# Optimization experiments

Measured on AMD Instinct MI355X. Metric: run time of the kernel, lower is better.

## Reference

```python
import jax, jax.numpy as jnp
import numpy as np

K = 3            # kernel size
C_IN = 8
C_OUT = 16
PATCH = C_IN * K * K  # 72
EPS = 1e-6


def setup_inputs() -> dict:
    key = jax.random.key(0)
    k1, k2, k3 = jax.random.split(key, 3)
    in_tensor = jax.random.normal(k1, (4, C_IN, 112, 112), dtype=jnp.float32)
    # 1x1-conv weighting predictor: C_in -> PATCH*C_OUT channels
    w_pred = jax.random.normal(k2, (PATCH * C_OUT, C_IN), dtype=jnp.float32) * 0.05
    b_pred = jax.random.normal(k3, (PATCH * C_OUT,), dtype=jnp.float32) * 0.05
    return {"in_tensor": in_tensor, "w_pred": w_pred, "b_pred": b_pred}


def reference(in_tensor, w_pred, b_pred):
    B, C, H, W = in_tensor.shape
    # --- weighting module: predict dynamic weights per spatial location ---
    raw = jnp.einsum('bchw,oc->bohw', in_tensor, w_pred) + b_pred[None, :, None, None]
    weightings = raw.reshape(B, PATCH, C_OUT, H, W)          # [B, C*k*k, C_out, H, W]
    # norm = L2 norm of the dynamic weight over the patch dim -> [B, C_out, H, W]
    norm = jnp.sqrt(jnp.sum(weightings * weightings, axis=1)) + EPS
    # --- unfold: overlapping k x k patches, same padding, stride 1 ---
    patches = jax.lax.conv_general_dilated_patches(
        in_tensor, (K, K), (1, 1), 'SAME')                   # [B, C*k*k, H, W]
    # --- weighted sum over the patch dim, then normalize ---
    activations = jnp.einsum('bphw,bpohw->bohw', patches, weightings)  # [B, C_out, H, W]
    return activations / norm
```

## Files before the change

kernel.cpp:

```cpp
#include <hip/hip_runtime.h>
#include <math.h>

#define IMG_W 112
#define HW    12544
#define CI    8
#define CO    16
#define NP2   36
#define EPS   1e-6f

typedef __attribute__((ext_vector_type(8))) short short8;
typedef __attribute__((ext_vector_type(16))) float f32x16;

static __device__ inline short f2bf(float f) {
  unsigned u = __float_as_uint(f);
  return (short)((u + 0x7FFFu + ((u >> 16) & 1u)) >> 16);
}

static constexpr int DQ[9] = {-113, -112, -111, -1, 0, 1, 111, 112, 113};

__global__ __launch_bounds__(256, 3) void coda_mfma(
    const float* __restrict__ in, const float* __restrict__ wp,
    const float* __restrict__ bp, float* __restrict__ out)
{
  __shared__ short sA[NP2][2][32][8];
  __shared__ float sBuf[CI * 290];

  const int tid = threadIdx.x;
  const int b   = blockIdx.x / 196;
  const int r0  = (blockIdx.x - b * 196) * 64;
  const float* __restrict__ inb = in + b * CI * HW;

  for (int idx = tid; idx < NP2 * 64; idx += 256) {
    const int p2 = idx >> 6, l = idx & 63, ah = l >> 5, m = l & 31;
    const int row = p2 * 32 + m;
    short8 v = {0, 0, 0, 0, 0, 0, 0, 0};
    if (ah == 0) {
      const float* wr = wp + row * CI;
#pragma unroll
      for (int j = 0; j < 8; ++j) v[j] = f2bf(wr[j]);
    } else {
      v[0] = f2bf(bp[row]);
    }
    *(short8*)&sA[p2][ah][m][0] = v;
  }
  for (int k = tid; k < CI * 290; k += 256) {
    const int c = k / 290;
    const int i = k - c * 290;
    int gg = r0 - 113 + i;
    gg = (gg < 0) ? 0 : (gg > HW - 1 ? HW - 1 : gg);
    sBuf[k] = inb[c * HW + gg];
  }
  __syncthreads();

  const int wave = tid >> 6;
  const int lane = tid & 63;
  const int g    = wave & 1;
  const int hh   = wave >> 1;
  const int ln   = lane & 31;
  const int hi   = lane >> 5;
  const int px   = r0 + g * 32 + ln;
  const int hrow = px / IMG_W;
  const int wcol = px - hrow * IMG_W;
  const int off  = g * 32 + ln + 113;

  float vm[9];
#pragma unroll
  for (int q = 0; q < 9; ++q) {
    const int kh = q / 3, kw = q % 3;
    const bool ok = ((unsigned)(hrow + kh - 1) < 112u) &&
                    ((unsigned)(wcol + kw - 1) < 112u);
    vm[q] = ok ? 1.f : 0.f;
  }

  short8 bf;
#pragma unroll
  for (int j = 0; j < 8; ++j) {
    const short bv = f2bf(sBuf[j * 290 + off]);
    bf[j] = (hi == 0) ? bv : ((j == 0) ? (short)0x3F80 : (short)0);
  }

  float acc[8] = {0.f, 0.f, 0.f, 0.f, 0.f, 0.f, 0.f, 0.f};
  float n2[8]  = {0.f, 0.f, 0.f, 0.f, 0.f, 0.f, 0.f, 0.f};

#pragma unroll
  for (int t = 0; t < 18; ++t) {
    const int c0_ = 4 * hh + (2 * t) / 9;
    const int q0_ = (2 * t) % 9;
    const int c1_ = 4 * hh + (2 * t + 1) / 9;
    const int q1_ = (2 * t + 1) % 9;

    const short8 af = *(const short8*)&sA[hh * 18 + t][hi][ln][0];
    const float pv0 = vm[q0_] * sBuf[c0_ * 290 + off + DQ[q0_]];
    const float pv1 = vm[q1_] * sBuf[c1_ * 290 + off + DQ[q1_]];

    const f32x16 zc = {0.f, 0.f, 0.f, 0.f, 0.f, 0.f, 0.f, 0.f,
                       0.f, 0.f, 0.f, 0.f, 0.f, 0.f, 0.f, 0.f};
    const f32x16 d =
        __builtin_amdgcn_mfma_f32_32x32x16_bf16(af, bf, zc, 0, 0, 0);
#pragma unroll
    for (int i = 0; i < 16; ++i) {
      const float pv = (i < 8) ? pv0 : pv1;
      acc[i & 7] = fmaf(pv, d[i], acc[i & 7]);
      n2[i & 7]  = fmaf(d[i], d[i], n2[i & 7]);
    }
  }

  __syncthreads();
  if (hh == 1) {
#pragma unroll
    for (int j = 0; j < 8; ++j) {
      sBuf[j * 128 + g * 64 + lane]       = acc[j];
      sBuf[(j + 8) * 128 + g * 64 + lane] = n2[j];
    }
  }
  __syncthreads();
  if (hh == 0) {
    float* __restrict__ ob = out + (long)b * CO * HW + px;
#pragma unroll
    for (int j = 0; j < 8; ++j) {
      const float a2 = acc[j] + sBuf[j * 128 + g * 64 + lane];
      const float s2 = n2[j] + sBuf[(j + 8) * 128 + g * 64 + lane];
      const int co = (j & 3) + 8 * (j >> 2) + 4 * hi;
      ob[(long)co * HW] = a2 / (sqrtf(s2) + EPS);
    }
  }
}

extern "C" void kernel_launch(void* const* d_in, const int* in_sizes, int n_in,
                              void* d_out, int out_size, void* d_ws, size_t ws_size,
                              hipStream_t stream) {
  const float* in = (const float*)d_in[0];
  const float* wp = (const float*)d_in[1];
  const float* bp = (const float*)d_in[2];
  float* out = (float*)d_out;

  coda_mfma<<<dim3(784), dim3(256), 0, stream>>>(in, wp, bp, out);
}
```

Before: 77.09 us.

## Prepack bf16 weights in a separate kernel and read inputs directly from global

```diff
diff --git a/kernel.cpp b/kernel.cpp
--- a/kernel.cpp
+++ b/kernel.cpp
@@ -18,39 +18,35 @@
 
 static constexpr int DQ[9] = {-113, -112, -111, -1, 0, 1, 111, 112, 113};
 
-__global__ __launch_bounds__(256, 3) void coda_mfma(
-    const float* __restrict__ in, const float* __restrict__ wp,
-    const float* __restrict__ bp, float* __restrict__ out)
+__global__ __launch_bounds__(256) void coda_pack(
+    const float* __restrict__ wp, const float* __restrict__ bp,
+    short* __restrict__ wpk)
 {
-  __shared__ short sA[NP2][2][32][8];
-  __shared__ float sBuf[CI * 290];
+  const int t = blockIdx.x * 256 + threadIdx.x;
+  if (t >= NP2 * 64) return;
+  const int p2 = t >> 6, l = t & 63, ah = l >> 5, m = l & 31;
+  const int row = p2 * 32 + m;
+  short8 v = {0, 0, 0, 0, 0, 0, 0, 0};
+  if (ah == 0) {
+    const float* wr = wp + row * CI;
+#pragma unroll
+    for (int j = 0; j < 8; ++j) v[j] = f2bf(wr[j]);
+  } else {
+    v[0] = f2bf(bp[row]);
+  }
+  *(short8*)&wpk[t * 8] = v;
+}
+
+__global__ __launch_bounds__(256, 4) void coda_mfma(
+    const float* __restrict__ in, const short* __restrict__ wpk,
+    float* __restrict__ out)
+{
+  __shared__ float sPart[2 * 16 * 64];
 
   const int tid = threadIdx.x;
   const int b   = blockIdx.x / 196;
   const int r0  = (blockIdx.x - b * 196) * 64;
   const float* __restrict__ inb = in + b * CI * HW;
-
-  for (int idx = tid; idx < NP2 * 64; idx += 256) {
-    const int p2 = idx >> 6, l = idx & 63, ah = l >> 5, m = l & 31;
-    const int row = p2 * 32 + m;
-    short8 v = {0, 0, 0, 0, 0, 0, 0, 0};
-    if (ah == 0) {
-      const float* wr = wp + row * CI;
-#pragma unroll
-      for (int j = 0; j < 8; ++j) v[j] = f2bf(wr[j]);
-    } else {
-      v[0] = f2bf(bp[row]);
-    }
-    *(short8*)&sA[p2][ah][m][0] = v;
-  }
-  for (int k = tid; k < CI * 290; k += 256) {
-    const int c = k / 290;
-    const int i = k - c * 290;
-    int gg = r0 - 113 + i;
-    gg = (gg < 0) ? 0 : (gg > HW - 1 ? HW - 1 : gg);
-    sBuf[k] = inb[c * HW + gg];
-  }
-  __syncthreads();
 
   const int wave = tid >> 6;
   const int lane = tid & 63;
@@ -61,7 +57,6 @@
   const int px   = r0 + g * 32 + ln;
   const int hrow = px / IMG_W;
   const int wcol = px - hrow * IMG_W;
-  const int off  = g * 32 + ln + 113;
 
   float vm[9];
 #pragma unroll
@@ -75,23 +70,27 @@
   short8 bf;
 #pragma unroll
   for (int j = 0; j < 8; ++j) {
-    const short bv = f2bf(sBuf[j * 290 + off]);
+    const short bv = f2bf(inb[j * HW + px]);
     bf[j] = (hi == 0) ? bv : ((j == 0) ? (short)0x3F80 : (short)0);
   }
 
   float acc[8] = {0.f, 0.f, 0.f, 0.f, 0.f, 0.f, 0.f, 0.f};
   float n2[8]  = {0.f, 0.f, 0.f, 0.f, 0.f, 0.f, 0.f, 0.f};
 
+  const short* __restrict__ wbase = wpk + (hh * 18 * 64 + lane) * 8;
+
 #pragma unroll
   for (int t = 0; t < 18; ++t) {
-    const int c0_ = 4 * hh + (2 * t) / 9;
-    const int q0_ = (2 * t) % 9;
-    const int c1_ = 4 * hh + (2 * t + 1) / 9;
-    const int q1_ = (2 * t + 1) % 9;
+    const int p0  = 36 * hh + 2 * t;
+    const int c0_ = p0 / 9,       q0_ = p0 % 9;
+    const int c1_ = (p0 + 1) / 9, q1_ = (p0 + 1) % 9;
 
-    const short8 af = *(const short8*)&sA[hh * 18 + t][hi][ln][0];
-    const float pv0 = vm[q0_] * sBuf[c0_ * 290 + off + DQ[q0_]];
-    const float pv1 = vm[q1_] * sBuf[c1_ * 290 + off + DQ[q1_]];
+    const short8 af = *(const short8*)(wbase + t * 512);
+
+    int i0 = px + DQ[q0_]; i0 = i0 < 0 ? 0 : (i0 > HW - 1 ? HW - 1 : i0);
+    int i1 = px + DQ[q1_]; i1 = i1 < 0 ? 0 : (i1 > HW - 1 ? HW - 1 : i1);
+    const float pv0 = vm[q0_] * inb[c0_ * HW + i0];
+    const float pv1 = vm[q1_] * inb[c1_ * HW + i1];
 
     const f32x16 zc = {0.f, 0.f, 0.f, 0.f, 0.f, 0.f, 0.f, 0.f,
                        0.f, 0.f, 0.f, 0.f, 0.f, 0.f, 0.f, 0.f};
@@ -105,12 +104,11 @@
     }
   }
 
-  __syncthreads();
   if (hh == 1) {
 #pragma unroll
     for (int j = 0; j < 8; ++j) {
-      sBuf[j * 128 + g * 64 + lane]       = acc[j];
-      sBuf[(j + 8) * 128 + g * 64 + lane] = n2[j];
+      sPart[(g * 16 + j) * 64 + lane]     = acc[j];
+      sPart[(g * 16 + j + 8) * 64 + lane] = n2[j];
     }
   }
   __syncthreads();
@@ -118,8 +116,8 @@
     float* __restrict__ ob = out + (long)b * CO * HW + px;
 #pragma unroll
     for (int j = 0; j < 8; ++j) {
-      const float a2 = acc[j] + sBuf[j * 128 + g * 64 + lane];
-      const float s2 = n2[j] + sBuf[(j + 8) * 128 + g * 64 + lane];
+      const float a2 = acc[j] + sPart[(g * 16 + j) * 64 + lane];
+      const float s2 = n2[j] + sPart[(g * 16 + j + 8) * 64 + lane];
       const int co = (j & 3) + 8 * (j >> 2) + 4 * hi;
       ob[(long)co * HW] = a2 / (sqrtf(s2) + EPS);
     }
@@ -133,6 +131,8 @@
   const float* wp = (const float*)d_in[1];
   const float* bp = (const float*)d_in[2];
   float* out = (float*)d_out;
+  short* wpk = (short*)d_ws;
 
-  coda_mfma<<<dim3(784), dim3(256), 0, stream>>>(in, wp, bp, out);
+  coda_pack<<<dim3(9), dim3(256), 0, stream>>>(wp, bp, wpk);
+  coda_mfma<<<dim3(784), dim3(256), 0, stream>>>(in, wpk, out);
 }
```

Result: faster. 72.60 us (-5.8%).
